# Optimization experiments

Measured on AMD Instinct MI355X. Metric: run time of the kernel, lower is better.

The kernel has to match this reference:

```python
import jax, jax.numpy as jnp
import numpy as np

B, S, V, E, H, C = 64, 256, 50000, 512, 512, 20


def _lstm_dir(x, w_ih, w_hh, b_ih, b_hh):
    # x: [B,S,E]; PyTorch gate order i,f,g,o; returns hidden seq [B,S,H]
    h_dim = w_hh.shape[1]
    xproj = jnp.einsum('bse,ge->bsg', x, w_ih) + b_ih  # [B,S,4H]
    h0 = jnp.zeros((x.shape[0], h_dim), x.dtype)

    def step(carry, xt):
        h, c = carry
        g = xt + h @ w_hh.T + b_hh
        i, f, gg, o = jnp.split(g, 4, axis=-1)
        c = jax.nn.sigmoid(f) * c + jax.nn.sigmoid(i) * jnp.tanh(gg)
        h = jax.nn.sigmoid(o) * jnp.tanh(c)
        return (h, c), h

    _, hs = jax.lax.scan(step, (h0, h0), jnp.swapaxes(xproj, 0, 1))
    return jnp.swapaxes(hs, 0, 1)  # [B,S,H]


def setup_inputs() -> dict:
    key = jax.random.key(0)
    ks = jax.random.split(key, 16)
    sc = lambda fan: 1.0 / np.sqrt(fan)
    return {
        'x': jax.random.randint(ks[0], (B, S), 0, V),
        'embed': jax.random.normal(ks[1], (V, E), jnp.float32),
        'w_ih_f': jax.random.normal(ks[2], (4 * H, E), jnp.float32) * sc(E),
        'w_hh_f': jax.random.normal(ks[3], (4 * H, H), jnp.float32) * sc(H),
        'b_ih_f': jax.random.normal(ks[4], (4 * H,), jnp.float32) * sc(H),
        'b_hh_f': jax.random.normal(ks[5], (4 * H,), jnp.float32) * sc(H),
        'w_ih_b': jax.random.normal(ks[6], (4 * H, E), jnp.float32) * sc(E),
        'w_hh_b': jax.random.normal(ks[7], (4 * H, H), jnp.float32) * sc(H),
        'b_ih_b': jax.random.normal(ks[8], (4 * H,), jnp.float32) * sc(H),
        'b_hh_b': jax.random.normal(ks[9], (4 * H,), jnp.float32) * sc(H),
        'myw': jax.random.normal(ks[10], (2 * H, 1), jnp.float32),
        'lin1_w': jax.random.normal(ks[11], (H, 2 * H), jnp.float32) * sc(2 * H),
        'lin1_b': jax.random.normal(ks[12], (H,), jnp.float32) * sc(2 * H),
        'lin2_w': jax.random.normal(ks[13], (C, H), jnp.float32) * sc(H),
        'lin2_b': jax.random.normal(ks[14], (C,), jnp.float32) * sc(H),
    }


def reference(x, embed, w_ih_f, w_hh_f, b_ih_f, b_hh_f,
              w_ih_b, w_hh_b, b_ih_b, b_hh_b,
              myw, lin1_w, lin1_b, lin2_w, lin2_b):
    emb = embed[x]                                   # [B,S,E] (dropout=eval no-op)
    h_f = _lstm_dir(emb, w_ih_f, w_hh_f, b_ih_f, b_hh_f)
    h_b = _lstm_dir(emb[:, ::-1], w_ih_b, w_hh_b, b_ih_b, b_hh_b)[:, ::-1]
    out = jnp.concatenate([h_f, h_b], axis=-1)       # [B,S,2H]
    # additive-ish attention: weights = exp(tanh(h . w)), normalized by row sum
    p = jnp.exp(jnp.tanh(jnp.einsum('bsd,d->bs', out, myw[:, 0])))  # [B,S]
    denom = jax.lax.stop_gradient(p.sum(axis=1, keepdims=True))     # .data in torch
    pooled = jnp.einsum('bs,bsd->bd', p / denom, out)               # [B,2H]
    h1 = pooled @ lin1_w.T + lin1_b
    return h1 @ lin2_w.T + lin2_b                     # [B,C]
```

## Files before the change

kernel.cpp:

```cpp
#include <hip/hip_runtime.h>

typedef _Float16 f16;
typedef _Float16 half8 __attribute__((ext_vector_type(8)));
typedef float floatx4 __attribute__((ext_vector_type(4)));
typedef unsigned long long u64;
typedef unsigned int u32;
typedef unsigned int u32v4 __attribute__((ext_vector_type(4)));

#define NB 64
#define NS 256
#define NE 512
#define NH 512
#define NG 2048
#define NN 4096

#define OFF_XP     0
#define OFF_EMB    134217728
#define OFF_WCAT   150994944
#define OFF_WHH    155189248
#define OFF_HSEQ   159383552
#define OFF_BIAS   193200128
#define OFF_HEXT   OFF_EMB

__device__ __forceinline__ void cbar() {
  asm volatile("" ::: "memory");
}
__device__ __forceinline__ float fast_tanh(float x) {
  float e = __expf(2.f * x);
  return 1.f - 2.f / (1.f + e);
}

__global__ void k_prep(float* bias,
                       const float* bihf, const float* bhhf,
                       const float* bihb, const float* bhhb) {
  int id = blockIdx.x * 256 + threadIdx.x;
  bias[id] = (id < 2048) ? (bihf[id] + bhhf[id]) : (bihb[id - 2048] + bhhb[id - 2048]);
}

__global__ void k_zero(uint4* p) {
  uint4 z; z.x = 0; z.y = 0; z.z = 0; z.w = 0;
  p[blockIdx.x * 256 + threadIdx.x] = z;
}

__global__ void k_embed(const int* __restrict__ x, const float* __restrict__ embed,
                        f16* __restrict__ emb_h) {
  int gid = blockIdx.x * 256 + threadIdx.x;
  size_t base = (size_t)gid * 8;
  int r = (int)(base >> 9);
  int e = (int)(base & 511);
  int xi = x[r];
  const float4* src = (const float4*)(embed + (size_t)xi * 512 + e);
  float4 a = src[0], b = src[1];
  half8 h;
  h[0] = (f16)a.x; h[1] = (f16)a.y; h[2] = (f16)a.z; h[3] = (f16)a.w;
  h[4] = (f16)b.x; h[5] = (f16)b.y; h[6] = (f16)b.z; h[7] = (f16)b.w;
  *(half8*)(emb_h + base) = h;
}

__global__ void k_wcast(const float* __restrict__ wihf, const float* __restrict__ wihb,
                        const float* __restrict__ whhf, const float* __restrict__ whhb,
                        f16* __restrict__ w_cat, f16* __restrict__ whh) {
  int gid = blockIdx.x * 256 + threadIdx.x;
  size_t i8 = (size_t)gid * 8;
  const float* src;
  f16* dst;
  if (i8 < 2097152) {
    size_t n = i8 >> 9, k = i8 & 511;
    src = (n < 2048 ? wihf + n * 512 : wihb + (n - 2048) * 512) + k;
    dst = w_cat + i8;
  } else {
    size_t i2 = i8 - 2097152;
    int dir = (int)(i2 >> 20);
    size_t rk = i2 & 1048575;
    src = (dir ? whhb : whhf) + rk;
    dst = whh + i2;
  }
  float4 a = *(const float4*)src, b = *(const float4*)(src + 4);
  half8 h;
  h[0] = (f16)a.x; h[1] = (f16)a.y; h[2] = (f16)a.z; h[3] = (f16)a.w;
  h[4] = (f16)b.x; h[5] = (f16)b.y; h[6] = (f16)b.z; h[7] = (f16)b.w;
  *(half8*)dst = h;
}

__global__ __launch_bounds__(256) void k_gemm(const f16* __restrict__ A,
                                              const f16* __restrict__ Bw,
                                              const float* __restrict__ bias,
                                              f16* __restrict__ xp) {
  __shared__ __align__(16) f16 As[128 * 32];
  __shared__ __align__(16) f16 Bs[128 * 32];
  const int t = threadIdx.x;
  const int m0 = blockIdx.x * 128;
  const int n0 = blockIdx.y * 128;
  const int w = t >> 6, l = t & 63;
  const int wm = w >> 1, wn = w & 1;
  const int l15 = l & 15, q8 = (l >> 4) * 8;

  floatx4 acc[4][4];
#pragma unroll
  for (int mi = 0; mi < 4; mi++)
#pragma unroll
    for (int ni = 0; ni < 4; ni++) {
      acc[mi][ni][0] = 0.f; acc[mi][ni][1] = 0.f;
      acc[mi][ni][2] = 0.f; acc[mi][ni][3] = 0.f;
    }

  for (int kt = 0; kt < 16; kt++) {
#pragma unroll
    for (int i = 0; i < 2; i++) {
      int c = t + 256 * i;
      int row = c >> 2, kc = (c & 3) * 8;
      *(uint4*)&As[row * 32 + kc] = *(const uint4*)(A + (size_t)(m0 + row) * 512 + kt * 32 + kc);
      *(uint4*)&Bs[row * 32 + kc] = *(const uint4*)(Bw + (size_t)(n0 + row) * 512 + kt * 32 + kc);
    }
    __syncthreads();
    half8 af[4], bf[4];
#pragma unroll
    for (int mi = 0; mi < 4; mi++)
      af[mi] = *(const half8*)&As[(wm * 64 + mi * 16 + l15) * 32 + q8];
#pragma unroll
    for (int ni = 0; ni < 4; ni++)
      bf[ni] = *(const half8*)&Bs[(wn * 64 + ni * 16 + l15) * 32 + q8];
#pragma unroll
    for (int mi = 0; mi < 4; mi++)
#pragma unroll
      for (int ni = 0; ni < 4; ni++)
        acc[mi][ni] = __builtin_amdgcn_mfma_f32_16x16x32_f16(af[mi], bf[ni], acc[mi][ni], 0, 0, 0);
    __syncthreads();
  }

#pragma unroll
  for (int ni = 0; ni < 4; ni++) {
    int ng = n0 + wn * 64 + ni * 16 + l15;
    float bv = bias[ng];
#pragma unroll
    for (int mi = 0; mi < 4; mi++) {
      int mg = m0 + wm * 64 + mi * 16 + (l >> 4) * 4;
#pragma unroll
      for (int r = 0; r < 4; r++)
        xp[(size_t)(mg + r) * 4096 + ng] = (f16)(acc[mi][ni][r] + bv);
    }
  }
}

__global__ __launch_bounds__(256) void k_rec(const f16* __restrict__ whh,
                                             const f16* __restrict__ xp,
                                             u32* __restrict__ h_ext,
                                             f16* __restrict__ h_seq) {
  const int blk = blockIdx.x;
  const int dir = blk & 1;
  const int bg  = (blk >> 1) & 7;
  const int jg  = blk >> 4;
  const int t = threadIdx.x;
  const int w = t >> 6, l = t & 63;
  const int l15 = l & 15, q = l >> 4;
  const int lb = l15 & 7;

  half8 fa[2][16];
  {
    const f16* wb = whh + ((size_t)dir * 2048 + w * 512 + jg * 32 + l15) * 512;
#pragma unroll
    for (int mi = 0; mi < 2; mi++)
#pragma unroll
      for (int kt = 0; kt < 16; kt++)
        fa[mi][kt] = *(const half8*)(wb + (size_t)mi * 16 * 512 + kt * 32 + q * 8);
  }

  __shared__ __align__(16) f16 hbuf[16 * 264];
  __shared__ float zbuf[4][32][19];
  __shared__ __align__(16) f16 hstage[8][32];

  float creg = 0.f;
  const int uhu = t & 31, ub = t >> 5;

  const size_t xrowb = ((size_t)(8 * bg + lb) * 256) * (size_t)NN +
                       (size_t)dir * 2048 + w * 512 + jg * 32 + q * 4;

  const int slab_rd_base = (dir * 8 + bg) * 4096;
  const int cl_b = t >> 5;
  const int cl_i = t & 31;
  const int cl_src32 = cl_b * 512 + cl_i * 16;
  const int cl_kt = cl_i >> 1;
  const int cl_sel = (cl_i & 1) * 16;
  const int cl_dst = cl_kt * 264 + cl_b * 32 + cl_sel;
  const int pub_idx = ub * 512 + jg * 32 + uhu;

#pragma unroll 1
  for (int st = 0; st < NS; st++) {
    const int s = dir ? (255 - st) : st;

    const f16* xpp = xp + xrowb + (size_t)s * NN;
    uint2 xv0 = *(const uint2*)xpp;
    uint2 xv1 = *(const uint2*)(xpp + 16);
    cbar();

    {
      const u32* slab32 = h_ext + ((st & 1) * 16 * 4096) + slab_rd_base;
      const u64* sp = (const u64*)(slab32 + cl_src32);
      const u64 tmask = 0xffff0000ffff0000ull;
      const u64 texp = ((u64)(u32)st << 16) | ((u64)(u32)st << 48);
      u64 wv0, wv1, wv2, wv3, wv4, wv5, wv6, wv7;
      while (true) {
        wv0 = __hip_atomic_load(sp + 0, __ATOMIC_RELAXED, __HIP_MEMORY_SCOPE_SYSTEM);
        wv1 = __hip_atomic_load(sp + 1, __ATOMIC_RELAXED, __HIP_MEMORY_SCOPE_SYSTEM);
        wv2 = __hip_atomic_load(sp + 2, __ATOMIC_RELAXED, __HIP_MEMORY_SCOPE_SYSTEM);
        wv3 = __hip_atomic_load(sp + 3, __ATOMIC_RELAXED, __HIP_MEMORY_SCOPE_SYSTEM);
        wv4 = __hip_atomic_load(sp + 4, __ATOMIC_RELAXED, __HIP_MEMORY_SCOPE_SYSTEM);
        wv5 = __hip_atomic_load(sp + 5, __ATOMIC_RELAXED, __HIP_MEMORY_SCOPE_SYSTEM);
        wv6 = __hip_atomic_load(sp + 6, __ATOMIC_RELAXED, __HIP_MEMORY_SCOPE_SYSTEM);
        wv7 = __hip_atomic_load(sp + 7, __ATOMIC_RELAXED, __HIP_MEMORY_SCOPE_SYSTEM);
        bool ok = ((wv0 & tmask) == texp) & ((wv1 & tmask) == texp) &
                  ((wv2 & tmask) == texp) & ((wv3 & tmask) == texp) &
                  ((wv4 & tmask) == texp) & ((wv5 & tmask) == texp) &
                  ((wv6 & tmask) == texp) & ((wv7 & tmask) == texp);
        if (ok) break;
        __builtin_amdgcn_s_sleep(1);
      }
      u32v4 d0, d1;
      d0[0] = (u32)(wv0 & 0xffffu) | ((u32)((wv0 >> 32) & 0xffffu) << 16);
      d0[1] = (u32)(wv1 & 0xffffu) | ((u32)((wv1 >> 32) & 0xffffu) << 16);
      d0[2] = (u32)(wv2 & 0xffffu) | ((u32)((wv2 >> 32) & 0xffffu) << 16);
      d0[3] = (u32)(wv3 & 0xffffu) | ((u32)((wv3 >> 32) & 0xffffu) << 16);
      d1[0] = (u32)(wv4 & 0xffffu) | ((u32)((wv4 >> 32) & 0xffffu) << 16);
      d1[1] = (u32)(wv5 & 0xffffu) | ((u32)((wv5 >> 32) & 0xffffu) << 16);
      d1[2] = (u32)(wv6 & 0xffffu) | ((u32)((wv6 >> 32) & 0xffffu) << 16);
      d1[3] = (u32)(wv7 & 0xffffu) | ((u32)((wv7 >> 32) & 0xffffu) << 16);
      *(u32v4*)&hbuf[cl_dst + 0] = d0;
      *(u32v4*)&hbuf[cl_dst + 8] = d1;
    }
    __syncthreads();

    floatx4 a0e, a0o, a1e, a1o;
    a0e[0]=0.f;a0e[1]=0.f;a0e[2]=0.f;a0e[3]=0.f;
    a0o[0]=0.f;a0o[1]=0.f;a0o[2]=0.f;a0o[3]=0.f;
    a1e[0]=0.f;a1e[1]=0.f;a1e[2]=0.f;a1e[3]=0.f;
    a1o[0]=0.f;a1o[1]=0.f;a1o[2]=0.f;a1o[3]=0.f;
#pragma unroll
    for (int kt = 0; kt < 16; kt += 2) {
      half8 bf0 = *(const half8*)&hbuf[kt * 264 + lb * 32 + q * 8];
      half8 bf1 = *(const half8*)&hbuf[(kt + 1) * 264 + lb * 32 + q * 8];
      a0e = __builtin_amdgcn_mfma_f32_16x16x32_f16(fa[0][kt], bf0, a0e, 0, 0, 0);
      a1e = __builtin_amdgcn_mfma_f32_16x16x32_f16(fa[1][kt], bf0, a1e, 0, 0, 0);
      a0o = __builtin_amdgcn_mfma_f32_16x16x32_f16(fa[0][kt + 1], bf1, a0o, 0, 0, 0);
      a1o = __builtin_amdgcn_mfma_f32_16x16x32_f16(fa[1][kt + 1], bf1, a1o, 0, 0, 0);
    }
    floatx4 acc0 = a0e + a0o;
    floatx4 acc1 = a1e + a1o;

    {
      const f16* x0 = (const f16*)&xv0;
      const f16* x1 = (const f16*)&xv1;
#pragma unroll
      for (int r = 0; r < 4; r++) {
        zbuf[w][q * 4 + r][l15]      = acc0[r] + (float)x0[r];
        zbuf[w][16 + q * 4 + r][l15] = acc1[r] + (float)x1[r];
      }
    }
    __syncthreads();

    {
      float iv = zbuf[0][uhu][ub];
      float fv = zbuf[1][uhu][ub];
      float gv = zbuf[2][uhu][ub];
      float ov = zbuf[3][uhu][ub];
      float ig = 1.f / (1.f + __expf(-iv));
      float fg = 1.f / (1.f + __expf(-fv));
      float og = 1.f / (1.f + __expf(-ov));
      creg = fg * creg + ig * fast_tanh(gv);
      f16 hh = (f16)(og * fast_tanh(creg));
      unsigned short hb = __builtin_bit_cast(unsigned short, hh);
      u32 word = (u32)hb | ((u32)(st + 1) << 16);
      u32* wslab = h_ext + (((st + 1) & 1) * 16 * 4096) + slab_rd_base;
      __hip_atomic_store(wslab + pub_idx, word, __ATOMIC_RELAXED,
                         __HIP_MEMORY_SCOPE_SYSTEM);
      hstage[ub][uhu] = hh;
    }
    __syncthreads();

    if (t < 64) {
      const int pb = t >> 3, pc = (t & 7) * 4;
      u64 hv = *(const u64*)&hstage[pb][pc];
      *(u64*)(h_seq + ((size_t)(8 * bg + pb) * 256 + s) * 1024 + dir * 512 + jg * 32 + pc) = hv;
    }
  }
}

__global__ __launch_bounds__(256) void k_attn(const f16* __restrict__ h_seq,
                                              const float* __restrict__ myw,
                                              const float* __restrict__ l1w,
                                              const float* __restrict__ l1b,
                                              const float* __restrict__ l2w,
                                              const float* __restrict__ l2b,
                                              float* __restrict__ out) {
  const int b = blockIdx.x;
  const int t = threadIdx.x;
  const int w = t >> 6, l = t & 63;
  float mw[16];
#pragma unroll
  for (int i = 0; i < 16; i += 4) {
    float4 v = *(const float4*)(myw + l * 16 + i);
    mw[i] = v.x; mw[i + 1] = v.y; mw[i + 2] = v.z; mw[i + 3] = v.w;
  }
  float pool[16];
#pragma unroll
  for (int i = 0; i < 16; i++) pool[i] = 0.f;
  float psum = 0.f;

  for (int s = w; s < NS; s += 4) {
    const f16* hp = h_seq + ((size_t)b * NS + s) * 1024 + l * 16;
    half8 h0 = *(const half8*)hp;
    half8 h1 = *(const half8*)(hp + 8);
    float hv[16];
#pragma unroll
    for (int i = 0; i < 8; i++) { hv[i] = (float)h0[i]; hv[8 + i] = (float)h1[i]; }
    float d = 0.f;
#pragma unroll
    for (int i = 0; i < 16; i++) d += hv[i] * mw[i];
#pragma unroll
    for (int off = 32; off > 0; off >>= 1) d += __shfl_xor(d, off);
    float p = __expf(tanhf(d));
    psum += p;
#pragma unroll
    for (int i = 0; i < 16; i++) pool[i] += p * hv[i];
  }

  __shared__ float zb[4][1024];
  __shared__ float ps[4];
  __shared__ float pooled[1024];
  __shared__ float h1s[512];
#pragma unroll
  for (int i = 0; i < 16; i++) zb[w][l * 16 + i] = pool[i];
  if (l == 0) ps[w] = psum;
  __syncthreads();
  float denom = ps[0] + ps[1] + ps[2] + ps[3];
  for (int d0 = t; d0 < 1024; d0 += 256)
    pooled[d0] = (zb[0][d0] + zb[1][d0] + zb[2][d0] + zb[3][d0]) / denom;
  __syncthreads();
  for (int r = t; r < 512; r += 256) {
    const float* wr = l1w + (size_t)r * 1024;
    float a = l1b[r];
    for (int k = 0; k < 1024; k += 4) {
      float4 wv = *(const float4*)(wr + k);
      a += wv.x * pooled[k] + wv.y * pooled[k + 1] + wv.z * pooled[k + 2] + wv.w * pooled[k + 3];
    }
    h1s[r] = a;
  }
  __syncthreads();
  if (t < 20) {
    const float* wr = l2w + t * 512;
    float a = l2b[t];
    for (int k = 0; k < 512; k++) a += h1s[k] * wr[k];
    out[b * 20 + t] = a;
  }
}

extern "C" void kernel_launch(void* const* d_in, const int* in_sizes, int n_in,
                              void* d_out, int out_size, void* d_ws, size_t ws_size,
                              hipStream_t stream) {
  (void)in_sizes; (void)n_in; (void)out_size; (void)ws_size;
  const int*   x     = (const int*)d_in[0];
  const float* embed = (const float*)d_in[1];
  const float* wihf  = (const float*)d_in[2];
  const float* whhf  = (const float*)d_in[3];
  const float* bihf  = (const float*)d_in[4];
  const float* bhhf  = (const float*)d_in[5];
  const float* wihb  = (const float*)d_in[6];
  const float* whhb  = (const float*)d_in[7];
  const float* bihb  = (const float*)d_in[8];
  const float* bhhb  = (const float*)d_in[9];
  const float* myw   = (const float*)d_in[10];
  const float* l1w   = (const float*)d_in[11];
  const float* l1b   = (const float*)d_in[12];
  const float* l2w   = (const float*)d_in[13];
  const float* l2b   = (const float*)d_in[14];

  char* ws = (char*)d_ws;
  f16*   xp    = (f16*)(ws + OFF_XP);
  f16*   emb_h = (f16*)(ws + OFF_EMB);
  f16*   w_cat = (f16*)(ws + OFF_WCAT);
  f16*   whh   = (f16*)(ws + OFF_WHH);
  f16*   h_seq = (f16*)(ws + OFF_HSEQ);
  u32*   h_ext = (u32*)(ws + OFF_HEXT);
  float* bias  = (float*)(ws + OFF_BIAS);
  float* out   = (float*)d_out;

  k_prep<<<16, 256, 0, stream>>>(bias, bihf, bhhf, bihb, bhhb);
  k_embed<<<4096, 256, 0, stream>>>(x, embed, emb_h);
  k_wcast<<<2048, 256, 0, stream>>>(wihf, wihb, whhf, whhb, w_cat, whh);
  k_gemm<<<dim3(128, 32), 256, 0, stream>>>(emb_h, w_cat, bias, xp);
  k_zero<<<128, 256, 0, stream>>>((uint4*)(ws + OFF_HEXT));
  k_rec<<<256, 256, 0, stream>>>(whh, xp, h_ext, h_seq);
  k_attn<<<64, 256, 0, stream>>>(h_seq, myw, l1w, l1b, l2w, l2b, out);
}
```

Before: 1.034 ms.

## Remap gate rows per wave to drop block barriers in LSTM recurrence

Reassigns the W_hh rows each wave holds so that one wave owns all four gates (i,f,g,o) for 8 hidden units. The gate combine can then read only that wave's own shared-memory tile after a wave-level barrier, replacing two block-wide __syncthreads per step. The h buffer is double-buffered by step parity so the next step's writes cannot race with reads from the current step. The spin-wait now keeps two sets of loads in flight, and h_seq is written directly per thread as scattered 2-byte stores instead of through a staging buffer, which costs some store efficiency.

```diff
diff --git a/kernel.cpp b/kernel.cpp
--- a/kernel.cpp
+++ b/kernel.cpp
@@ -28,6 +28,9 @@
 __device__ __forceinline__ float fast_tanh(float x) {
   float e = __expf(2.f * x);
   return 1.f - 2.f / (1.f + e);
+}
+__device__ __forceinline__ u64 sysld(const u64* p) {
+  return __hip_atomic_load(p, __ATOMIC_RELAXED, __HIP_MEMORY_SCOPE_SYSTEM);
 }
 
 __global__ void k_prep(float* bias,
@@ -153,79 +156,85 @@
   const int t = threadIdx.x;
   const int w = t >> 6, l = t & 63;
   const int l15 = l & 15, q = l >> 4;
-  const int lb = l15 & 7;
+  const int lb = l & 7;
 
   half8 fa[2][16];
   {
-    const f16* wb = whh + ((size_t)dir * 2048 + w * 512 + jg * 32 + l15) * 512;
-#pragma unroll
-    for (int mi = 0; mi < 2; mi++)
+#pragma unroll
+    for (int mi = 0; mi < 2; mi++) {
+      const int gate = 2 * mi + (l15 >> 3);
+      const f16* wb = whh + ((size_t)dir * 2048 + gate * 512 + jg * 32 + w * 8 + (l15 & 7)) * 512;
 #pragma unroll
       for (int kt = 0; kt < 16; kt++)
-        fa[mi][kt] = *(const half8*)(wb + (size_t)mi * 16 * 512 + kt * 32 + q * 8);
-  }
-
-  __shared__ __align__(16) f16 hbuf[16 * 264];
-  __shared__ float zbuf[4][32][19];
-  __shared__ __align__(16) f16 hstage[8][32];
-
+        fa[mi][kt] = *(const half8*)(wb + kt * 32 + q * 8);
+    }
+  }
+
+  __shared__ __align__(16) f16 hbuf[2][16 * 264];
+  __shared__ float zw[4][32][18];
   float creg = 0.f;
-  const int uhu = t & 31, ub = t >> 5;
-
-  const size_t xrowb = ((size_t)(8 * bg + lb) * 256) * (size_t)NN +
-                       (size_t)dir * 2048 + w * 512 + jg * 32 + q * 4;
+
+  const int cb = l >> 3, cu = l & 7;
+
+  const size_t xrow = ((size_t)(8 * bg + lb) * 256);
+  const int xc0 = dir * 2048 + (q >> 1) * 512 + jg * 32 + w * 8 + (q & 1) * 4;
+  const int xc1 = xc0 + 1024;
 
   const int slab_rd_base = (dir * 8 + bg) * 4096;
   const int cl_b = t >> 5;
   const int cl_i = t & 31;
   const int cl_src32 = cl_b * 512 + cl_i * 16;
-  const int cl_kt = cl_i >> 1;
-  const int cl_sel = (cl_i & 1) * 16;
-  const int cl_dst = cl_kt * 264 + cl_b * 32 + cl_sel;
-  const int pub_idx = ub * 512 + jg * 32 + uhu;
+  const int cl_dst = (cl_i >> 1) * 264 + cl_b * 32 + (cl_i & 1) * 16;
+  const int pub_idx = cb * 512 + jg * 32 + w * 8 + cu;
 
 #pragma unroll 1
   for (int st = 0; st < NS; st++) {
     const int s = dir ? (255 - st) : st;
-
-    const f16* xpp = xp + xrowb + (size_t)s * NN;
-    uint2 xv0 = *(const uint2*)xpp;
-    uint2 xv1 = *(const uint2*)(xpp + 16);
+    const int p = st & 1;
+
+    uint2 xv0 = *(const uint2*)(xp + (xrow + s) * NN + xc0);
+    uint2 xv1 = *(const uint2*)(xp + (xrow + s) * NN + xc1);
     cbar();
 
     {
-      const u32* slab32 = h_ext + ((st & 1) * 16 * 4096) + slab_rd_base;
+      const u32* slab32 = h_ext + (p * 16 * 4096) + slab_rd_base;
       const u64* sp = (const u64*)(slab32 + cl_src32);
       const u64 tmask = 0xffff0000ffff0000ull;
       const u64 texp = ((u64)(u32)st << 16) | ((u64)(u32)st << 48);
-      u64 wv0, wv1, wv2, wv3, wv4, wv5, wv6, wv7;
+      u64 w0, w1, w2, w3, w4, w5, w6, w7;
+      u64 a0 = sysld(sp + 0), a1 = sysld(sp + 1), a2 = sysld(sp + 2), a3 = sysld(sp + 3);
+      u64 a4 = sysld(sp + 4), a5 = sysld(sp + 5), a6 = sysld(sp + 6), a7 = sysld(sp + 7);
       while (true) {
-        wv0 = __hip_atomic_load(sp + 0, __ATOMIC_RELAXED, __HIP_MEMORY_SCOPE_SYSTEM);
-        wv1 = __hip_atomic_load(sp + 1, __ATOMIC_RELAXED, __HIP_MEMORY_SCOPE_SYSTEM);
-        wv2 = __hip_atomic_load(sp + 2, __ATOMIC_RELAXED, __HIP_MEMORY_SCOPE_SYSTEM);
-        wv3 = __hip_atomic_load(sp + 3, __ATOMIC_RELAXED, __HIP_MEMORY_SCOPE_SYSTEM);
-        wv4 = __hip_atomic_load(sp + 4, __ATOMIC_RELAXED, __HIP_MEMORY_SCOPE_SYSTEM);
-        wv5 = __hip_atomic_load(sp + 5, __ATOMIC_RELAXED, __HIP_MEMORY_SCOPE_SYSTEM);
-        wv6 = __hip_atomic_load(sp + 6, __ATOMIC_RELAXED, __HIP_MEMORY_SCOPE_SYSTEM);
-        wv7 = __hip_atomic_load(sp + 7, __ATOMIC_RELAXED, __HIP_MEMORY_SCOPE_SYSTEM);
-        bool ok = ((wv0 & tmask) == texp) & ((wv1 & tmask) == texp) &
-                  ((wv2 & tmask) == texp) & ((wv3 & tmask) == texp) &
-                  ((wv4 & tmask) == texp) & ((wv5 & tmask) == texp) &
-                  ((wv6 & tmask) == texp) & ((wv7 & tmask) == texp);
-        if (ok) break;
-        __builtin_amdgcn_s_sleep(1);
+        u64 b0 = sysld(sp + 0), b1 = sysld(sp + 1), b2 = sysld(sp + 2), b3 = sysld(sp + 3);
+        u64 b4 = sysld(sp + 4), b5 = sysld(sp + 5), b6 = sysld(sp + 6), b7 = sysld(sp + 7);
+        if (((a0 & tmask) == texp) & ((a1 & tmask) == texp) &
+            ((a2 & tmask) == texp) & ((a3 & tmask) == texp) &
+            ((a4 & tmask) == texp) & ((a5 & tmask) == texp) &
+            ((a6 & tmask) == texp) & ((a7 & tmask) == texp)) {
+          w0 = a0; w1 = a1; w2 = a2; w3 = a3; w4 = a4; w5 = a5; w6 = a6; w7 = a7;
+          break;
+        }
+        a0 = sysld(sp + 0); a1 = sysld(sp + 1); a2 = sysld(sp + 2); a3 = sysld(sp + 3);
+        a4 = sysld(sp + 4); a5 = sysld(sp + 5); a6 = sysld(sp + 6); a7 = sysld(sp + 7);
+        if (((b0 & tmask) == texp) & ((b1 & tmask) == texp) &
+            ((b2 & tmask) == texp) & ((b3 & tmask) == texp) &
+            ((b4 & tmask) == texp) & ((b5 & tmask) == texp) &
+            ((b6 & tmask) == texp) & ((b7 & tmask) == texp)) {
+          w0 = b0; w1 = b1; w2 = b2; w3 = b3; w4 = b4; w5 = b5; w6 = b6; w7 = b7;
+          break;
+        }
       }
       u32v4 d0, d1;
-      d0[0] = (u32)(wv0 & 0xffffu) | ((u32)((wv0 >> 32) & 0xffffu) << 16);
-      d0[1] = (u32)(wv1 & 0xffffu) | ((u32)((wv1 >> 32) & 0xffffu) << 16);
-      d0[2] = (u32)(wv2 & 0xffffu) | ((u32)((wv2 >> 32) & 0xffffu) << 16);
-      d0[3] = (u32)(wv3 & 0xffffu) | ((u32)((wv3 >> 32) & 0xffffu) << 16);
-      d1[0] = (u32)(wv4 & 0xffffu) | ((u32)((wv4 >> 32) & 0xffffu) << 16);
-      d1[1] = (u32)(wv5 & 0xffffu) | ((u32)((wv5 >> 32) & 0xffffu) << 16);
-      d1[2] = (u32)(wv6 & 0xffffu) | ((u32)((wv6 >> 32) & 0xffffu) << 16);
-      d1[3] = (u32)(wv7 & 0xffffu) | ((u32)((wv7 >> 32) & 0xffffu) << 16);
-      *(u32v4*)&hbuf[cl_dst + 0] = d0;
-      *(u32v4*)&hbuf[cl_dst + 8] = d1;
+      d0[0] = (u32)(w0 & 0xffffu) | ((u32)((w0 >> 32) & 0xffffu) << 16);
+      d0[1] = (u32)(w1 & 0xffffu) | ((u32)((w1 >> 32) & 0xffffu) << 16);
+      d0[2] = (u32)(w2 & 0xffffu) | ((u32)((w2 >> 32) & 0xffffu) << 16);
+      d0[3] = (u32)(w3 & 0xffffu) | ((u32)((w3 >> 32) & 0xffffu) << 16);
+      d1[0] = (u32)(w4 & 0xffffu) | ((u32)((w4 >> 32) & 0xffffu) << 16);
+      d1[1] = (u32)(w5 & 0xffffu) | ((u32)((w5 >> 32) & 0xffffu) << 16);
+      d1[2] = (u32)(w6 & 0xffffu) | ((u32)((w6 >> 32) & 0xffffu) << 16);
+      d1[3] = (u32)(w7 & 0xffffu) | ((u32)((w7 >> 32) & 0xffffu) << 16);
+      *(u32v4*)&hbuf[p][cl_dst + 0] = d0;
+      *(u32v4*)&hbuf[p][cl_dst + 8] = d1;
     }
     __syncthreads();
 
@@ -236,8 +245,8 @@
     a1o[0]=0.f;a1o[1]=0.f;a1o[2]=0.f;a1o[3]=0.f;
 #pragma unroll
     for (int kt = 0; kt < 16; kt += 2) {
-      half8 bf0 = *(const half8*)&hbuf[kt * 264 + lb * 32 + q * 8];
-      half8 bf1 = *(const half8*)&hbuf[(kt + 1) * 264 + lb * 32 + q * 8];
+      half8 bf0 = *(const half8*)&hbuf[p][kt * 264 + lb * 32 + q * 8];
+      half8 bf1 = *(const half8*)&hbuf[p][(kt + 1) * 264 + lb * 32 + q * 8];
       a0e = __builtin_amdgcn_mfma_f32_16x16x32_f16(fa[0][kt], bf0, a0e, 0, 0, 0);
       a1e = __builtin_amdgcn_mfma_f32_16x16x32_f16(fa[1][kt], bf0, a1e, 0, 0, 0);
       a0o = __builtin_amdgcn_mfma_f32_16x16x32_f16(fa[0][kt + 1], bf1, a0o, 0, 0, 0);
@@ -251,17 +260,20 @@
       const f16* x1 = (const f16*)&xv1;
 #pragma unroll
       for (int r = 0; r < 4; r++) {
-        zbuf[w][q * 4 + r][l15]      = acc0[r] + (float)x0[r];
-        zbuf[w][16 + q * 4 + r][l15] = acc1[r] + (float)x1[r];
+        zw[w][q * 4 + r][l15]      = acc0[r] + (float)x0[r];
+        zw[w][16 + q * 4 + r][l15] = acc1[r] + (float)x1[r];
       }
     }
-    __syncthreads();
+    cbar();
+    __builtin_amdgcn_wave_barrier();
+    asm volatile("s_waitcnt lgkmcnt(0)" ::: "memory");
+    __builtin_amdgcn_sched_barrier(0);
 
     {
-      float iv = zbuf[0][uhu][ub];
-      float fv = zbuf[1][uhu][ub];
-      float gv = zbuf[2][uhu][ub];
-      float ov = zbuf[3][uhu][ub];
+      float iv = zw[w][cu][cb];
+      float fv = zw[w][8 + cu][cb];
+      float gv = zw[w][16 + cu][cb];
+      float ov = zw[w][24 + cu][cb];
       float ig = 1.f / (1.f + __expf(-iv));
       float fg = 1.f / (1.f + __expf(-fv));
       float og = 1.f / (1.f + __expf(-ov));
@@ -272,14 +284,7 @@
       u32* wslab = h_ext + (((st + 1) & 1) * 16 * 4096) + slab_rd_base;
       __hip_atomic_store(wslab + pub_idx, word, __ATOMIC_RELAXED,
                          __HIP_MEMORY_SCOPE_SYSTEM);
-      hstage[ub][uhu] = hh;
-    }
-    __syncthreads();
-
-    if (t < 64) {
-      const int pb = t >> 3, pc = (t & 7) * 4;
-      u64 hv = *(const u64*)&hstage[pb][pc];
-      *(u64*)(h_seq + ((size_t)(8 * bg + pb) * 256 + s) * 1024 + dir * 512 + jg * 32 + pc) = hv;
+      h_seq[((size_t)(8 * bg + cb) * 256 + s) * 1024 + dir * 512 + jg * 32 + w * 8 + cu] = hh;
     }
   }
 }
```

After: 1.547 ms. 1.5x slower.
